# Performance work log

Measured on AMD Instinct MI355X. Metric: run time of the kernel, lower is better.

The kernel has to match this reference:

```python
import jax, jax.numpy as jnp
import numpy as np

B, IN, OUT, K = 512, 65536, 16384, 32

def setup_inputs() -> dict:
    key = jax.random.key(0)
    k1, k2, k3 = jax.random.split(key, 3)
    x = jax.random.normal(k1, (B, IN), dtype=jnp.float32)
    indices = jax.random.randint(k2, (OUT, K), 0, IN, dtype=jnp.int32)
    weight = jax.random.normal(k3, (OUT, K), dtype=jnp.float32) * 0.1
    bias = jnp.zeros((OUT,), dtype=jnp.float32)
    return {"x": x, "indices": indices, "weight": weight, "bias": bias}

def reference(x, indices, weight, bias):
    # Gather per-output feature subsets: (B, OUT, K)
    x_sel = x[:, indices]
    # Weighted sum over K connections per output, plus bias: (B, OUT)
    out = jnp.einsum('bok,ok->bo', x_sel, weight) + bias
    return out
```

## Files before the change

### kernel.cpp

```cpp
#include <hip/hip_runtime.h>

#define B_DIM   512
#define IN_DIM  65536
#define OUT_DIM 16384
#define K_DIM   32

static __device__ __forceinline__ unsigned short f2bf(float f) {
    unsigned u = __builtin_bit_cast(unsigned, f);
    unsigned r = (u + 0x7FFFu + ((u >> 16) & 1u)) >> 16;
    return (unsigned short)r;
}

static __device__ __forceinline__ float fcomp(float4 v, int c) {
    switch (c & 3) { case 0: return v.x; case 1: return v.y; case 2: return v.z; default: return v.w; }
}

__global__ __launch_bounds__(256) void transpose_bf16_k(const float* __restrict__ x,
                                                        unsigned short* __restrict__ xT) {
    const int c0 = blockIdx.x * 16;
    const int t  = threadIdx.x;
    #pragma unroll
    for (int h = 0; h < 2; ++h) {
        const int b = h * 256 + t;
        const float4* p = (const float4*)(x + (size_t)b * IN_DIM + c0);
        float4 v0 = p[0], v1 = p[1], v2 = p[2], v3 = p[3];
        #pragma unroll
        for (int c = 0; c < 16; ++c) {
            const float4 vv = (c < 4) ? v0 : (c < 8) ? v1 : (c < 12) ? v2 : v3;
            xT[(size_t)(c0 + c) * B_DIM + b] = f2bf(fcomp(vv, c));
        }
    }
}

#define SE 520

static __device__ __forceinline__ int icomp(int4 v, int c) {
    switch (c & 3) { case 0: return v.x; case 1: return v.y; case 2: return v.z; default: return v.w; }
}

__global__ __launch_bounds__(128, 4) void sparse_main(const unsigned short* __restrict__ xT,
                                                      const int*   __restrict__ idxp,
                                                      const float* __restrict__ wp,
                                                      const float* __restrict__ biasp,
                                                      float*       __restrict__ out) {
    __shared__ float lds[8][SE];
    const int o_blk = blockIdx.x * 8;
    const int t    = threadIdx.x;
    const int lane = t & 63;
    const int b4   = t * 4;

    const int4   iv = ((const int4*)  (idxp + o_blk * K_DIM))[lane];
    const float4 wv = ((const float4*)(wp   + o_blk * K_DIM))[lane];

    float4 acc[8];
    #pragma unroll
    for (int o = 0; o < 8; ++o) acc[o] = make_float4(0.f, 0.f, 0.f, 0.f);

    #pragma unroll
    for (int o = 0; o < 8; ++o) {
        #pragma unroll
        for (int k = 0; k < K_DIM; ++k) {
            const int flat = o * K_DIM + k;
            const int sl   = flat >> 2;
            const int   sidx = __builtin_amdgcn_readlane(icomp(iv, flat), sl);
            const float sw   = __int_as_float(
                __builtin_amdgcn_readlane(__float_as_int(fcomp(wv, flat)), sl));
            const uint2 u = *(const uint2*)(xT + ((size_t)sidx << 9) + b4);
            acc[o].x = fmaf(sw, __int_as_float(u.x << 16),          acc[o].x);
            acc[o].y = fmaf(sw, __int_as_float(u.x & 0xFFFF0000u),  acc[o].y);
            acc[o].z = fmaf(sw, __int_as_float(u.y << 16),          acc[o].z);
            acc[o].w = fmaf(sw, __int_as_float(u.y & 0xFFFF0000u),  acc[o].w);
        }
    }

    #pragma unroll
    for (int o = 0; o < 8; ++o) {
        const float bv = biasp[o_blk + o];
        acc[o].x += bv; acc[o].y += bv; acc[o].z += bv; acc[o].w += bv;
        *(float4*)(&lds[o][b4]) = acc[o];
    }
    __syncthreads();

    #pragma unroll
    for (int p = 0; p < 8; ++p) {
        const int q = p * 512 + t * 4;
        const int b = q >> 3;
        const int o = q & 7;
        float4 v;
        v.x = lds[o + 0][b];
        v.y = lds[o + 1][b];
        v.z = lds[o + 2][b];
        v.w = lds[o + 3][b];
        *(float4*)(out + (size_t)b * OUT_DIM + o_blk + o) = v;
    }
}

__global__ void sparse_fallback(const float* __restrict__ x,
                                const int*   __restrict__ idxp,
                                const float* __restrict__ wp,
                                const float* __restrict__ biasp,
                                float*       __restrict__ out) {
    const int i = blockIdx.x * blockDim.x + threadIdx.x;
    if (i >= B_DIM * OUT_DIM) return;
    const int b = i / OUT_DIM;
    const int o = i % OUT_DIM;
    float a = biasp[o];
    for (int k = 0; k < K_DIM; ++k) {
        const int idx = idxp[o * K_DIM + k];
        a = fmaf(wp[o * K_DIM + k], x[(size_t)b * IN_DIM + idx], a);
    }
    out[i] = a;
}

extern "C" void kernel_launch(void* const* d_in, const int* in_sizes, int n_in,
                              void* d_out, int out_size, void* d_ws, size_t ws_size,
                              hipStream_t stream) {
    const float* x       = (const float*)d_in[0];
    const int*   indices = (const int*)  d_in[1];
    const float* weight  = (const float*)d_in[2];
    const float* bias    = (const float*)d_in[3];
    float*       out     = (float*)d_out;

    const size_t need = (size_t)IN_DIM * B_DIM * sizeof(unsigned short);
    if (ws_size >= need) {
        unsigned short* xT = (unsigned short*)d_ws;
        transpose_bf16_k<<<IN_DIM / 16, 256, 0, stream>>>(x, xT);
        sparse_main<<<OUT_DIM / 8, 128, 0, stream>>>(xT, indices, weight, bias, out);
    } else {
        const int n = B_DIM * OUT_DIM;
        sparse_fallback<<<(n + 255) / 256, 256, 0, stream>>>(x, indices, weight, bias, out);
    }
}
```

Baseline: 325.5 us.

## Stage each batch row in LDS as bf16 and gather from shared memory

Replaces the global transpose-to-bf16 plus gather kernels with a fused kernel where each block loads one batch row of x into LDS as bf16 and performs all sparse gathers from LDS. Indices and weights are pre-packed into 32-bit words (16-bit index, bf16 weight) to halve metadata traffic. This removes the 64 MB transposed intermediate and scattered global gathers, at the cost of re-reading the packed metadata per batch row from L2, low occupancy from 128 KB LDS per block, LDS bank conflicts, and bf16 rounding of the weights.

```diff
diff --git a/kernel.cpp b/kernel.cpp
--- a/kernel.cpp
+++ b/kernel.cpp
@@ -5,93 +5,68 @@
 #define OUT_DIM 16384
 #define K_DIM   32
 
-static __device__ __forceinline__ unsigned short f2bf(float f) {
+static __device__ __forceinline__ unsigned f2bf(float f) {
     unsigned u = __builtin_bit_cast(unsigned, f);
-    unsigned r = (u + 0x7FFFu + ((u >> 16) & 1u)) >> 16;
-    return (unsigned short)r;
+    return (u + 0x7FFFu + ((u >> 16) & 1u)) >> 16;
 }
 
-static __device__ __forceinline__ float fcomp(float4 v, int c) {
-    switch (c & 3) { case 0: return v.x; case 1: return v.y; case 2: return v.z; default: return v.w; }
+__global__ __launch_bounds__(256) void pack_k(const int* __restrict__ idxp,
+                                              const float* __restrict__ wp,
+                                              unsigned* __restrict__ packed) {
+    const int i = blockIdx.x * 256 + threadIdx.x;
+    const int4   iv = ((const int4*)idxp)[i];
+    const float4 wv = ((const float4*)wp)[i];
+    uint4 p;
+    p.x = ((unsigned)iv.x & 0xFFFFu) | (f2bf(wv.x) << 16);
+    p.y = ((unsigned)iv.y & 0xFFFFu) | (f2bf(wv.y) << 16);
+    p.z = ((unsigned)iv.z & 0xFFFFu) | (f2bf(wv.z) << 16);
+    p.w = ((unsigned)iv.w & 0xFFFFu) | (f2bf(wv.w) << 16);
+    ((uint4*)packed)[i] = p;
 }
 
-__global__ __launch_bounds__(256) void transpose_bf16_k(const float* __restrict__ x,
-                                                        unsigned short* __restrict__ xT) {
-    const int c0 = blockIdx.x * 16;
-    const int t  = threadIdx.x;
+__global__ __launch_bounds__(1024) void fused_k(const float* __restrict__ x,
+                                                const unsigned* __restrict__ packed,
+                                                const float* __restrict__ biasp,
+                                                float* __restrict__ out) {
+    __shared__ unsigned short xs[IN_DIM];
+    const int b = blockIdx.x;
+    const int t = threadIdx.x;
+
+    const float4* xr = (const float4*)(x + (size_t)b * IN_DIM);
+    unsigned* xs32 = (unsigned*)xs;
     #pragma unroll
-    for (int h = 0; h < 2; ++h) {
-        const int b = h * 256 + t;
-        const float4* p = (const float4*)(x + (size_t)b * IN_DIM + c0);
-        float4 v0 = p[0], v1 = p[1], v2 = p[2], v3 = p[3];
-        #pragma unroll
-        for (int c = 0; c < 16; ++c) {
-            const float4 vv = (c < 4) ? v0 : (c < 8) ? v1 : (c < 12) ? v2 : v3;
-            xT[(size_t)(c0 + c) * B_DIM + b] = f2bf(fcomp(vv, c));
-        }
-    }
-}
-
-#define SE 520
-
-static __device__ __forceinline__ int icomp(int4 v, int c) {
-    switch (c & 3) { case 0: return v.x; case 1: return v.y; case 2: return v.z; default: return v.w; }
-}
-
-__global__ __launch_bounds__(128, 4) void sparse_main(const unsigned short* __restrict__ xT,
-                                                      const int*   __restrict__ idxp,
-                                                      const float* __restrict__ wp,
-                                                      const float* __restrict__ biasp,
-                                                      float*       __restrict__ out) {
-    __shared__ float lds[8][SE];
-    const int o_blk = blockIdx.x * 8;
-    const int t    = threadIdx.x;
-    const int lane = t & 63;
-    const int b4   = t * 4;
-
-    const int4   iv = ((const int4*)  (idxp + o_blk * K_DIM))[lane];
-    const float4 wv = ((const float4*)(wp   + o_blk * K_DIM))[lane];
-
-    float4 acc[8];
-    #pragma unroll
-    for (int o = 0; o < 8; ++o) acc[o] = make_float4(0.f, 0.f, 0.f, 0.f);
-
-    #pragma unroll
-    for (int o = 0; o < 8; ++o) {
-        #pragma unroll
-        for (int k = 0; k < K_DIM; ++k) {
-            const int flat = o * K_DIM + k;
-            const int sl   = flat >> 2;
-            const int   sidx = __builtin_amdgcn_readlane(icomp(iv, flat), sl);
-            const float sw   = __int_as_float(
-                __builtin_amdgcn_readlane(__float_as_int(fcomp(wv, flat)), sl));
-            const uint2 u = *(const uint2*)(xT + ((size_t)sidx << 9) + b4);
-            acc[o].x = fmaf(sw, __int_as_float(u.x << 16),          acc[o].x);
-            acc[o].y = fmaf(sw, __int_as_float(u.x & 0xFFFF0000u),  acc[o].y);
-            acc[o].z = fmaf(sw, __int_as_float(u.y << 16),          acc[o].z);
-            acc[o].w = fmaf(sw, __int_as_float(u.y & 0xFFFF0000u),  acc[o].w);
-        }
-    }
-
-    #pragma unroll
-    for (int o = 0; o < 8; ++o) {
-        const float bv = biasp[o_blk + o];
-        acc[o].x += bv; acc[o].y += bv; acc[o].z += bv; acc[o].w += bv;
-        *(float4*)(&lds[o][b4]) = acc[o];
+    for (int j = 0; j < 16; ++j) {
+        const int e = j * 1024 + t;
+        float4 v = xr[e];
+        uint2 pkt;
+        pkt.x = f2bf(v.x) | (f2bf(v.y) << 16);
+        pkt.y = f2bf(v.z) | (f2bf(v.w) << 16);
+        *(uint2*)(xs32 + 2 * e) = pkt;
     }
     __syncthreads();
 
-    #pragma unroll
-    for (int p = 0; p < 8; ++p) {
-        const int q = p * 512 + t * 4;
-        const int b = q >> 3;
-        const int o = q & 7;
-        float4 v;
-        v.x = lds[o + 0][b];
-        v.y = lds[o + 1][b];
-        v.z = lds[o + 2][b];
-        v.w = lds[o + 3][b];
-        *(float4*)(out + (size_t)b * OUT_DIM + o_blk + o) = v;
+    #pragma unroll 2
+    for (int j = 0; j < 16; ++j) {
+        const int o = j * 1024 + t;
+        const uint4* pr = (const uint4*)(packed + (size_t)o * K_DIM);
+        uint4 q[8];
+        #pragma unroll
+        for (int c = 0; c < 8; ++c) q[c] = pr[c];
+
+        float acc = 0.f;
+        #pragma unroll
+        for (int c = 0; c < 8; ++c) {
+            const unsigned u0 = q[c].x, u1 = q[c].y, u2 = q[c].z, u3 = q[c].w;
+            acc = fmaf(__uint_as_float(u0 & 0xFFFF0000u),
+                       __uint_as_float(((unsigned)xs[u0 & 0xFFFFu]) << 16), acc);
+            acc = fmaf(__uint_as_float(u1 & 0xFFFF0000u),
+                       __uint_as_float(((unsigned)xs[u1 & 0xFFFFu]) << 16), acc);
+            acc = fmaf(__uint_as_float(u2 & 0xFFFF0000u),
+                       __uint_as_float(((unsigned)xs[u2 & 0xFFFFu]) << 16), acc);
+            acc = fmaf(__uint_as_float(u3 & 0xFFFF0000u),
+                       __uint_as_float(((unsigned)xs[u3 & 0xFFFFu]) << 16), acc);
+        }
+        out[(size_t)b * OUT_DIM + o] = acc + biasp[o];
     }
 }
 
@@ -121,11 +96,11 @@
     const float* bias    = (const float*)d_in[3];
     float*       out     = (float*)d_out;
 
-    const size_t need = (size_t)IN_DIM * B_DIM * sizeof(unsigned short);
+    const size_t need = (size_t)OUT_DIM * K_DIM * sizeof(unsigned);
     if (ws_size >= need) {
-        unsigned short* xT = (unsigned short*)d_ws;
-        transpose_bf16_k<<<IN_DIM / 16, 256, 0, stream>>>(x, xT);
-        sparse_main<<<OUT_DIM / 8, 128, 0, stream>>>(xT, indices, weight, bias, out);
+        unsigned* packed = (unsigned*)d_ws;
+        pack_k<<<(OUT_DIM * K_DIM / 4) / 256, 256, 0, stream>>>(indices, weight, packed);
+        fused_k<<<B_DIM, 1024, 0, stream>>>(x, packed, bias, out);
     } else {
         const int n = B_DIM * OUT_DIM;
         sparse_fallback<<<(n + 255) / 256, 256, 0, stream>>>(x, indices, weight, bias, out);
```

Result: slower. 356.2 us (+9.4%).
